# Kernel tuning notes

Hardware: AMD Instinct MI355X
Metric: run time of the kernel (lower is better)

## Reference

```python
import jax, jax.numpy as jnp
import numpy as np

N, E, IN_FEATS, D, H, DIST_DIM, NBOUND = 10000, 160000, 128, 64, 4, 32, 31

def setup_inputs() -> dict:
    key = jax.random.key(0)
    ks = jax.random.split(key, 16)
    gain = 5.0 / 3.0  # tanh gain
    def xavier(k, shape):
        # xavier_normal over the last two dims (fan_in, fan_out) as torch does per-slice
        fan_in, fan_out = shape[-2], shape[-1]
        std = gain * np.sqrt(2.0 / (fan_in + fan_out))
        return jax.random.normal(k, shape, dtype=jnp.float32) * std
    inp = {
        'feat': jax.random.normal(ks[0], (N, IN_FEATS), dtype=jnp.float32),
        'locations': jax.random.normal(ks[1], (N, 3), dtype=jnp.float32),
        'src': jax.random.randint(ks[2], (E,), 0, N),
        'dst': jax.random.randint(ks[3], (E,), 0, N),
        'inter_ids': jax.random.randint(ks[4], (E, H), 0, N),
        'W_fc': xavier(ks[5], (IN_FEATS, H * D)),
        'embed_table': jax.random.normal(ks[6], (NBOUND + 1, DIST_DIM), dtype=jnp.float32),
        'G': xavier(ks[7], (H, DIST_DIM, D)),
        'attn_fc1': xavier(ks[8], (H, 2 * D, D)),
        'attn_fc2': xavier(ks[9], (H, 2 * D, D)),
        'attn_fc3': xavier(ks[10], (H, 2 * D, D)),
        'attn_fc': xavier(ks[11], (H, 3 * D, D)),
        'attn_out': xavier(ks[12], (H, D, 1)),
        'boundaries': jnp.linspace(0.1, 3.1, NBOUND).astype(jnp.float32),
    }
    return inp


def reference(feat, locations, W_fc, embed_table, G, attn_fc1, attn_fc2, attn_fc3,
              attn_fc, attn_out, boundaries, src, dst, inter_ids):
    n = feat.shape[0]
    h = (feat @ W_fc).reshape(n, H, D)                      # [N,H,D]
    pos = locations                                          # [N,3]
    src_pos = pos[src]                                       # [E,3]
    dst_pos = pos[dst]                                       # [E,3]
    inter_pos = pos[inter_ids]                               # [E,H,3]
    h_src = h[src]                                           # [E,H,D]
    h_dst = h[dst]                                           # [E,H,D]
    head_idx = jnp.arange(H)[None, :]
    inter_h = h[inter_ids, head_idx, :]                      # [E,H,D] per-head gather

    e_count = src.shape[0]
    dist1 = jnp.broadcast_to(jnp.linalg.norm(dst_pos - src_pos, axis=-1)[:, None], (e_count, H))
    dist2 = jnp.linalg.norm(dst_pos[:, None, :] - inter_pos, axis=-1)   # [E,H]
    dist_ = jnp.linalg.norm(src_pos[:, None, :] - inter_pos, axis=-1)   # [E,H]

    def dist_embed(dist):
        idx = jnp.searchsorted(boundaries, dist, side='left')  # torch.bucketize(right=False)
        e = embed_table[idx]                                   # [E,H,DIST_DIM]
        return jnp.einsum('ehk,hkd->ehd', e, G)                # [E,H,D]

    de1 = dist_embed(dist1)
    de2 = dist_embed(dist2)
    de_ = dist_embed(dist_)

    d1 = jnp.einsum('ehk,hkd->ehd', jnp.concatenate([h_src, de1], axis=-1), attn_fc1)
    d2 = jnp.einsum('ehk,hkd->ehd', jnp.concatenate([inter_h, de2], axis=-1), attn_fc2)
    d3 = jnp.einsum('ehk,hkd->ehd', jnp.concatenate([h_dst, de_], axis=-1), attn_fc3)

    h_c = jnp.tanh(jnp.einsum('ehk,hkd->ehd', jnp.concatenate([d1, d2, d3], axis=-1), attn_fc))
    e_score = jnp.einsum('ehd,hdo->eho', h_c, attn_out)[..., 0]        # [E,H]

    # edge softmax grouped by destination node
    m = jax.ops.segment_max(e_score, dst, num_segments=n)              # [N,H]
    ex = jnp.exp(e_score - m[dst])
    den = jax.ops.segment_sum(ex, dst, num_segments=n)                 # [N,H]
    a = ex / den[dst]                                                  # [E,H]

    ft = jax.ops.segment_sum(a[:, :, None] * h_src, dst, num_segments=n)  # [N,H,D]
    rst = jnp.mean(ft, axis=1)                                          # merge='mean' -> [N,D]
    return rst
```

## Files before the change

### kernel.cpp

```cpp
#include <hip/hip_runtime.h>
#include <hip/hip_fp16.h>
#include <math.h>

#define N_NODES 10000
#define E_EDGES 160000
#define DMODEL 64
#define H 4
#define NBOUND 31
#define QREC 1024

typedef _Float16 half8 __attribute__((ext_vector_type(8)));
typedef float floatx4 __attribute__((ext_vector_type(4)));

__global__ __launch_bounds__(256) void prep_pre1_cvt_kernel(
    const float* __restrict__ fc1, const float* __restrict__ fc2,
    const float* __restrict__ fc3, const float* __restrict__ fcc,
    float* __restrict__ Bws, const float* __restrict__ pos,
    float4* __restrict__ pos4, int* __restrict__ counts,
    const float* __restrict__ feat, __half* __restrict__ feat16) {
  __shared__ __align__(16) float S[12288];
  int bi = blockIdx.x;
  int tid = threadIdx.x;
  if (bi >= 52) {
    int t = (bi - 52) * 256 + tid;
    float4 v = *(const float4*)(feat + t * 4);
    union { uint2 u; __half2 h[2]; } st;
    st.h[0] = __floats2half2_rn(v.x, v.y);
    st.h[1] = __floats2half2_rn(v.z, v.w);
    *(uint2*)&feat16[t * 4] = st.u;
    return;
  }
  if (bi >= 12) {
    int n = (bi - 12) * 256 + tid;
    if (n < N_NODES) {
      counts[n] = 0;
      pos4[n] = make_float4(pos[n * 3], pos[n * 3 + 1], pos[n * 3 + 2], 0.f);
    }
    return;
  }
  int kh = bi;
  int k = kh >> 2, h = kh & 3;
  const float* fck = (k == 0) ? fc1 : (k == 1) ? fc2 : fc3;
  fck += h * 128 * 64;
  const float* F = fcc + h * 192 * 64 + k * 64 * 64;
  #pragma unroll
  for (int u = 0; u < 8; ++u)
    ((float4*)S)[u * 256 + tid] = ((const float4*)fck)[u * 256 + tid];
  #pragma unroll
  for (int u = 0; u < 4; ++u)
    ((float4*)(S + 8192))[u * 256 + tid] = ((const float4*)F)[u * 256 + tid];
  __syncthreads();
  int j = tid & 63, ig = tid >> 6;
  #pragma unroll
  for (int rg = 0; rg < 8; ++rg) {
    int i0 = ig * 32 + rg * 4;
    float a0 = 0.f, a1 = 0.f, a2 = 0.f, a3 = 0.f;
    #pragma unroll
    for (int t4 = 0; t4 < 16; ++t4) {
      float4 f0 = *(const float4*)&S[(i0 + 0) * 64 + t4 * 4];
      float4 f1 = *(const float4*)&S[(i0 + 1) * 64 + t4 * 4];
      float4 f2 = *(const float4*)&S[(i0 + 2) * 64 + t4 * 4];
      float4 f3 = *(const float4*)&S[(i0 + 3) * 64 + t4 * 4];
      float b0 = S[8192 + (t4 * 4 + 0) * 64 + j];
      float b1 = S[8192 + (t4 * 4 + 1) * 64 + j];
      float b2 = S[8192 + (t4 * 4 + 2) * 64 + j];
      float b3 = S[8192 + (t4 * 4 + 3) * 64 + j];
      a0 += f0.x * b0 + f0.y * b1 + f0.z * b2 + f0.w * b3;
      a1 += f1.x * b0 + f1.y * b1 + f1.z * b2 + f1.w * b3;
      a2 += f2.x * b0 + f2.y * b1 + f2.z * b2 + f2.w * b3;
      a3 += f3.x * b0 + f3.y * b1 + f3.z * b2 + f3.w * b3;
    }
    Bws[kh * 8192 + (i0 + 0) * 64 + j] = a0;
    Bws[kh * 8192 + (i0 + 1) * 64 + j] = a1;
    Bws[kh * 8192 + (i0 + 2) * 64 + j] = a2;
    Bws[kh * 8192 + (i0 + 3) * 64 + j] = a3;
  }
}

__device__ __forceinline__ int didx(const float* __restrict__ bnd2, float d) {
  int g = (int)(d * 10.0f);
  g = (g < 0) ? 0 : ((g > 31) ? 31 : g);
  g += (bnd2[g + 1] < d) ? 1 : 0;
  g -= (bnd2[g] >= d) ? 1 : 0;
  return g;
}

__device__ __forceinline__ void dist_one(
    const float* __restrict__ S, const int* __restrict__ src,
    const int* __restrict__ dst, const int* __restrict__ inter,
    const float4* __restrict__ pos4, int* __restrict__ counts,
    int* __restrict__ widx, int g) {
  int e = g >> 2, h = g & 3;
  int s = src[e], t = dst[e];
  int it = inter[g];
  float4 ps = pos4[s], pt = pos4[t], pi = pos4[it];
  float dx = pt.x - ps.x, dy = pt.y - ps.y, dz = pt.z - ps.z;
  float dist1 = sqrtf(dx * dx + dy * dy + dz * dz);
  float ax = pt.x - pi.x, ay = pt.y - pi.y, az = pt.z - pi.z;
  float dist2 = sqrtf(ax * ax + ay * ay + az * az);
  float bx = ps.x - pi.x, by = ps.y - pi.y, bz = ps.z - pi.z;
  float dist_ = sqrtf(bx * bx + by * by + bz * bz);
  int idx1 = didx(S, dist1);
  int idx2 = didx(S, dist2);
  int idx_ = didx(S, dist_);
  widx[g] = idx1 | (idx2 << 5) | (idx_ << 10);
  if (h == 0) atomicAdd(&counts[t], 1);
}

__global__ __launch_bounds__(256) void pre2_dist_kernel(
    const float* __restrict__ Wfc, const float* __restrict__ G,
    const float* __restrict__ emb, const float* __restrict__ Bws,
    __half* __restrict__ bigWT, __half* __restrict__ U16,
    const int* __restrict__ src, const int* __restrict__ dst,
    const int* __restrict__ inter, const float4* __restrict__ pos4,
    const float* __restrict__ boundaries, int* __restrict__ counts,
    int* __restrict__ widx) {
  __shared__ __align__(16) float S[9216];
  int bi = blockIdx.x;
  int tid = threadIdx.x;
  if (bi >= 60) {
    if (tid < NBOUND) S[tid + 1] = boundaries[tid];
    if (tid == NBOUND) { S[0] = -INFINITY; S[32] = INFINITY; }
    __syncthreads();
    int g0 = (bi - 60) * 512 + tid;
    dist_one(S, src, dst, inter, pos4, counts, widx, g0);
    dist_one(S, src, dst, inter, pos4, counts, widx, g0 + 256);
    return;
  }
  int kh = bi / 5, role = bi % 5;
  int k = kh >> 2, h = kh & 3;
  int j = tid & 63;
  if (role < 4) {
    int r0 = role * 32;
    #pragma unroll
    for (int u = 0; u < 4; ++u)
      ((float4*)S)[u * 256 + tid] = ((const float4*)(Bws + kh * 8192))[u * 256 + tid];
    #pragma unroll
    for (int u = 0; u < 2; ++u) {
      int fi = u * 256 + tid;
      int i = fi >> 4, c4 = fi & 15;
      ((float4*)(S + 4096))[fi] =
          ((const float4*)(Wfc + (r0 + i) * 256 + h * 64))[c4];
    }
    __syncthreads();
    int ig = tid >> 6;
    int i0 = ig * 8;
    #pragma unroll
    for (int g4 = 0; g4 < 2; ++g4) {
      int ib = i0 + g4 * 4;
      float a0 = 0.f, a1 = 0.f, a2 = 0.f, a3 = 0.f;
      #pragma unroll
      for (int t4 = 0; t4 < 16; ++t4) {
        float4 f0 = *(const float4*)&S[4096 + (ib + 0) * 64 + t4 * 4];
        float4 f1 = *(const float4*)&S[4096 + (ib + 1) * 64 + t4 * 4];
        float4 f2 = *(const float4*)&S[4096 + (ib + 2) * 64 + t4 * 4];
        float4 f3 = *(const float4*)&S[4096 + (ib + 3) * 64 + t4 * 4];
        float b0 = S[(t4 * 4 + 0) * 64 + j];
        float b1 = S[(t4 * 4 + 1) * 64 + j];
        float b2 = S[(t4 * 4 + 2) * 64 + j];
        float b3 = S[(t4 * 4 + 3) * 64 + j];
        a0 += f0.x * b0 + f0.y * b1 + f0.z * b2 + f0.w * b3;
        a1 += f1.x * b0 + f1.y * b1 + f1.z * b2 + f1.w * b3;
        a2 += f2.x * b0 + f2.y * b1 + f2.z * b2 + f2.w * b3;
        a3 += f3.x * b0 + f3.y * b1 + f3.z * b2 + f3.w * b3;
      }
      __half hv[4] = {__float2half(a0), __float2half(a1), __float2half(a2),
                      __float2half(a3)};
      *(uint2*)&bigWT[((k + 1) * 256 + h * 64 + j) * 128 + r0 + ib] =
          *(uint2*)hv;
    }
    if (k == 0) {
      #pragma unroll
      for (int u = 0; u < 8; ++u) {
        int idx = u * 256 + tid;
        int i = idx >> 6, jj = idx & 63;
        bigWT[(h * 64 + jj) * 128 + r0 + i] = __float2half(S[4096 + idx]);
      }
    }
  } else {
    #pragma unroll
    for (int u = 0; u < 4; ++u)
      ((float4*)S)[u * 256 + tid] =
          ((const float4*)(Bws + kh * 8192 + 4096))[u * 256 + tid];
    #pragma unroll
    for (int u = 0; u < 2; ++u)
      ((float4*)(S + 4096))[u * 256 + tid] =
          ((const float4*)(G + h * 2048))[u * 256 + tid];
    ((float4*)(S + 6144))[tid] = ((const float4*)emb)[tid];
    __syncthreads();
    int wv = tid >> 6;
    #pragma unroll
    for (int rg = 0; rg < 2; ++rg) {
      int g0 = wv * 8 + rg * 4;
      float a0 = 0.f, a1 = 0.f, a2 = 0.f, a3 = 0.f;
      #pragma unroll
      for (int t4 = 0; t4 < 16; ++t4) {
        float4 f0 = *(const float4*)&S[4096 + (g0 + 0) * 64 + t4 * 4];
        float4 f1 = *(const float4*)&S[4096 + (g0 + 1) * 64 + t4 * 4];
        float4 f2 = *(const float4*)&S[4096 + (g0 + 2) * 64 + t4 * 4];
        float4 f3 = *(const float4*)&S[4096 + (g0 + 3) * 64 + t4 * 4];
        float b0 = S[(t4 * 4 + 0) * 64 + j];
        float b1 = S[(t4 * 4 + 1) * 64 + j];
        float b2 = S[(t4 * 4 + 2) * 64 + j];
        float b3 = S[(t4 * 4 + 3) * 64 + j];
        a0 += f0.x * b0 + f0.y * b1 + f0.z * b2 + f0.w * b3;
        a1 += f1.x * b0 + f1.y * b1 + f1.z * b2 + f1.w * b3;
        a2 += f2.x * b0 + f2.y * b1 + f2.z * b2 + f2.w * b3;
        a3 += f3.x * b0 + f3.y * b1 + f3.z * b2 + f3.w * b3;
      }
      S[7168 + (g0 + 0) * 64 + j] = a0;
      S[7168 + (g0 + 1) * 64 + j] = a1;
      S[7168 + (g0 + 2) * 64 + j] = a2;
      S[7168 + (g0 + 3) * 64 + j] = a3;
    }
    __syncthreads();
    #pragma unroll
    for (int rg = 0; rg < 2; ++rg) {
      int e0 = wv * 8 + rg * 4;
      float a0 = 0.f, a1 = 0.f, a2 = 0.f, a3 = 0.f;
      #pragma unroll
      for (int t4 = 0; t4 < 8; ++t4) {
        float4 f0 = *(const float4*)&S[6144 + (e0 + 0) * 32 + t4 * 4];
        float4 f1 = *(const float4*)&S[6144 + (e0 + 1) * 32 + t4 * 4];
        float4 f2 = *(const float4*)&S[6144 + (e0 + 2) * 32 + t4 * 4];
        float4 f3 = *(const float4*)&S[6144 + (e0 + 3) * 32 + t4 * 4];
        float b0 = S[7168 + (t4 * 4 + 0) * 64 + j];
        float b1 = S[7168 + (t4 * 4 + 1) * 64 + j];
        float b2 = S[7168 + (t4 * 4 + 2) * 64 + j];
        float b3 = S[7168 + (t4 * 4 + 3) * 64 + j];
        a0 += f0.x * b0 + f0.y * b1 + f0.z * b2 + f0.w * b3;
        a1 += f1.x * b0 + f1.y * b1 + f1.z * b2 + f1.w * b3;
        a2 += f2.x * b0 + f2.y * b1 + f2.z * b2 + f2.w * b3;
        a3 += f3.x * b0 + f3.y * b1 + f3.z * b2 + f3.w * b3;
      }
      int base = k * 8192 + h * 2048;
      U16[base + (e0 + 0) * 64 + j] = __float2half(a0);
      U16[base + (e0 + 1) * 64 + j] = __float2half(a1);
      U16[base + (e0 + 2) * 64 + j] = __float2half(a2);
      U16[base + (e0 + 3) * 64 + j] = __float2half(a3);
    }
  }
}

#define EROW 264

__global__ __launch_bounds__(256) void scan_gemm_kernel(
    const int* __restrict__ counts, int* __restrict__ starts,
    int* __restrict__ cursor, const __half* __restrict__ feat16,
    const __half* __restrict__ bigWT, __half* __restrict__ qall) {
  int bi = blockIdx.x;
  int tid = threadIdx.x;
  if (bi == 0) {
    __shared__ int lds[256];
    int base = tid * 40;
    int loc[40];
    int s = 0;
    #pragma unroll
    for (int u = 0; u < 40; ++u) {
      int i = base + u;
      int v = (i < N_NODES) ? counts[i] : 0;
      loc[u] = s;
      s += v;
    }
    lds[tid] = s;
    __syncthreads();
    int inc = s;
    for (int off = 1; off < 256; off <<= 1) {
      int y = (tid >= off) ? lds[tid - off] : 0;
      __syncthreads();
      inc += y;
      lds[tid] = inc;
      __syncthreads();
    }
    int excl = inc - s;
    #pragma unroll
    for (int u = 0; u < 40; ++u) {
      int i = base + u;
      if (i < N_NODES) {
        int v = excl + loc[u];
        starts[i] = v;
        cursor[i] = v;
      }
    }
    if (tid == 255) starts[N_NODES] = inc;
    return;
  }
  __shared__ __align__(16) __half Esm[4][16][EROW];
  int gb = bi - 1;
  int bx = gb % 157, by = gb / 157;
  int wv = tid >> 6, l = tid & 63;
  int m0 = bx * 64 + wv * 16;
  int n0 = by * 256;
  int lm = l & 15, lk = (l >> 4) * 8;
  int arow = m0 + lm;
  if (arow >= N_NODES) arow = N_NODES - 1;
  const _Float16* fp = (const _Float16*)feat16 + arow * 128 + lk;
  const _Float16* bp = (const _Float16*)bigWT + lk;
  half8 a[4];
  #pragma unroll
  for (int kt = 0; kt < 4; ++kt) a[kt] = *(const half8*)(fp + kt * 32);
  #pragma unroll
  for (int nt = 0; nt < 16; ++nt) {
    floatx4 acc = (floatx4){0.f, 0.f, 0.f, 0.f};
    #pragma unroll
    for (int kt = 0; kt < 4; ++kt) {
      half8 b = *(const half8*)(bp + (n0 + nt * 16 + lm) * 128 + kt * 32);
      acc = __builtin_amdgcn_mfma_f32_16x16x32_f16(a[kt], b, acc, 0, 0, 0);
    }
    int dd = nt * 16 + lm;
    int o = (by == 0) ? ((dd & 63) * 4 + (dd >> 6)) : dd;
    #pragma unroll
    for (int r4 = 0; r4 < 4; ++r4) {
      Esm[wv][(l >> 4) * 4 + r4][o] = __float2half(acc[r4]);
    }
  }
  __syncthreads();
  int row = l >> 2;
  int j0 = (l & 3) * 64;
  int m = m0 + row;
  if (m < N_NODES) {
    #pragma unroll
    for (int u = 0; u < 8; ++u) {
      uint4 v = *(const uint4*)&Esm[wv][row][j0 + u * 8];
      *(uint4*)&qall[m * QREC + by * 256 + j0 + u * 8] = v;
    }
  }
}

__device__ __forceinline__ float dpp_row_sum16(float v) {
  int x;
  x = __builtin_amdgcn_update_dpp(0, __float_as_int(v), 0x128, 0xf, 0xf, true);
  v += __int_as_float(x);
  x = __builtin_amdgcn_update_dpp(0, __float_as_int(v), 0x124, 0xf, 0xf, true);
  v += __int_as_float(x);
  x = __builtin_amdgcn_update_dpp(0, __float_as_int(v), 0x122, 0xf, 0xf, true);
  v += __int_as_float(x);
  x = __builtin_amdgcn_update_dpp(0, __float_as_int(v), 0x121, 0xf, 0xf, true);
  v += __int_as_float(x);
  return v;
}

union H4u { uint2 u; __half2 h[2]; };

__device__ __forceinline__ float tanh_dot(H4u A, H4u B, H4u C, H4u X, H4u Y,
                                          H4u Z, float4 a4) {
  __half2 z0 = __hadd2(__hadd2(A.h[0], B.h[0]), __hadd2(C.h[0], X.h[0]));
  z0 = __hadd2(z0, __hadd2(Y.h[0], Z.h[0]));
  __half2 z1 = __hadd2(__hadd2(A.h[1], B.h[1]), __hadd2(C.h[1], X.h[1]));
  z1 = __hadd2(z1, __hadd2(Y.h[1], Z.h[1]));
  float2 f0 = __half22float2(z0);
  float2 f1 = __half22float2(z1);
  const float K = 2.885390082f;
  float p0 = __builtin_amdgcn_exp2f(f0.x * K);
  float p1 = __builtin_amdgcn_exp2f(f0.y * K);
  float p2 = __builtin_amdgcn_exp2f(f1.x * K);
  float p3 = __builtin_amdgcn_exp2f(f1.y * K);
  float r0 = __builtin_amdgcn_rcpf(p0 + 1.0f);
  float r1 = __builtin_amdgcn_rcpf(p1 + 1.0f);
  float r2 = __builtin_amdgcn_rcpf(p2 + 1.0f);
  float r3 = __builtin_amdgcn_rcpf(p3 + 1.0f);
  float dot = a4.x * r0;
  dot = fmaf(a4.y, r1, dot);
  dot = fmaf(a4.z, r2, dot);
  dot = fmaf(a4.w, r3, dot);
  float asum = (a4.x + a4.y) + (a4.z + a4.w);
  return fmaf(-2.0f, dot, asum);
}

__global__ __launch_bounds__(256) void score_fill_kernel(
    const int* __restrict__ src, const int* __restrict__ dst,
    const int* __restrict__ inter, const int* __restrict__ widx,
    const __half* __restrict__ qall, const __half* __restrict__ U16,
    const float* __restrict__ aout, int* __restrict__ cursor,
    float* __restrict__ exsc, int* __restrict__ esrc) {
  int tid = threadIdx.x;
  int wv = tid >> 6, lane = tid & 63;
  int h = lane >> 4, c = lane & 15;
  int e0 = blockIdx.x * 8 + wv * 2;
  int e1 = e0 + 1;
  int s0 = src[e0], t0 = dst[e0];
  int s1 = src[e1], t1 = dst[e1];
  int it0 = inter[e0 * 4 + h], it1 = inter[e1 * 4 + h];
  int wp0 = widx[e0 * 4 + h], wp1 = widx[e1 * 4 + h];
  int i10 = wp0 & 31, i20 = (wp0 >> 5) & 31, i_0 = (wp0 >> 10) & 31;
  int i11 = wp1 & 31, i21 = (wp1 >> 5) & 31, i_1 = (wp1 >> 10) & 31;
  H4u A0, B0, C0, X0, Y0, Z0, A1, B1, C1, X1, Y1, Z1;
  A0.u = *(const uint2*)(qall + s0 * QREC + 256 + h * 64 + c * 4);
  A1.u = *(const uint2*)(qall + s1 * QREC + 256 + h * 64 + c * 4);
  B0.u = *(const uint2*)(qall + it0 * QREC + 512 + h * 64 + c * 4);
  B1.u = *(const uint2*)(qall + it1 * QREC + 512 + h * 64 + c * 4);
  C0.u = *(const uint2*)(qall + t0 * QREC + 768 + h * 64 + c * 4);
  C1.u = *(const uint2*)(qall + t1 * QREC + 768 + h * 64 + c * 4);
  X0.u = *(const uint2*)(U16 + (h * 32 + i10) * 64 + c * 4);
  X1.u = *(const uint2*)(U16 + (h * 32 + i11) * 64 + c * 4);
  Y0.u = *(const uint2*)(U16 + 8192 + (h * 32 + i20) * 64 + c * 4);
  Y1.u = *(const uint2*)(U16 + 8192 + (h * 32 + i21) * 64 + c * 4);
  Z0.u = *(const uint2*)(U16 + 16384 + (h * 32 + i_0) * 64 + c * 4);
  Z1.u = *(const uint2*)(U16 + 16384 + (h * 32 + i_1) * 64 + c * 4);
  const float4 a4 = *((const float4*)(aout + h * 64) + c);
  float v0 = tanh_dot(A0, B0, C0, X0, Y0, Z0, a4);
  float v1 = tanh_dot(A1, B1, C1, X1, Y1, Z1, a4);
  v0 = dpp_row_sum16(v0);
  v1 = dpp_row_sum16(v1);
  int p0 = 0, p1 = 0;
  if (lane == 0) {
    p0 = atomicAdd(&cursor[t0], 1);
    p1 = atomicAdd(&cursor[t1], 1);
  }
  p0 = __shfl(p0, 0);
  p1 = __shfl(p1, 0);
  if (c == 0) {
    exsc[p0 * 4 + h] = __expf(v0);
    exsc[p1 * 4 + h] = __expf(v1);
  }
  if (lane == 0) {
    esrc[p0] = s0;
    esrc[p1] = s1;
  }
}

__device__ __forceinline__ float4 h4_to_f4(uint2 u) {
  union { uint2 ui; __half2 h[2]; } cc;
  cc.ui = u;
  float2 a = __half22float2(cc.h[0]);
  float2 b = __half22float2(cc.h[1]);
  return make_float4(a.x, a.y, b.x, b.y);
}

__global__ __launch_bounds__(256) void agg_kernel(
    const int* __restrict__ starts, const int* __restrict__ esrc,
    const float* __restrict__ exsc, const __half* __restrict__ qall,
    float* __restrict__ out) {
  __shared__ float4 sm_num[4][64];
  __shared__ float4 sm_den[4];
  int tid = threadIdx.x;
  int w = tid >> 6, lane = tid & 63;
  int n = blockIdx.x;
  int b = starts[n], e_end = starts[n + 1];
  float4 num = make_float4(0.f, 0.f, 0.f, 0.f);
  float4 den = make_float4(0.f, 0.f, 0.f, 0.f);
  int i = b + w;
  while (i < e_end) {
    float4 ex[4];
    uint2 hr[4];
    #pragma unroll
    for (int u = 0; u < 4; ++u) {
      ex[u] = make_float4(0.f, 0.f, 0.f, 0.f);
      hr[u] = make_uint2(0, 0);
      int idx = i + u * 4;
      if (idx < e_end) {
        ex[u] = *(const float4*)(exsc + idx * 4);
        hr[u] = *(const uint2*)(qall + esrc[idx] * QREC + lane * 4);
      }
    }
    #pragma unroll
    for (int u = 0; u < 4; ++u) {
      float4 hv = h4_to_f4(hr[u]);
      num.x += ex[u].x * hv.x;
      num.y += ex[u].y * hv.y;
      num.z += ex[u].z * hv.z;
      num.w += ex[u].w * hv.w;
      den.x += ex[u].x; den.y += ex[u].y; den.z += ex[u].z; den.w += ex[u].w;
    }
    i += 16;
  }
  sm_num[w][lane] = num;
  if (lane == 0) sm_den[w] = den;
  __syncthreads();
  if (tid < 64) {
    float4 n0 = sm_num[0][tid], n1 = sm_num[1][tid];
    float4 n2 = sm_num[2][tid], n3 = sm_num[3][tid];
    float4 d0 = sm_den[0], d1 = sm_den[1], d2 = sm_den[2], d3 = sm_den[3];
    float4 ns = make_float4(n0.x + n1.x + n2.x + n3.x, n0.y + n1.y + n2.y + n3.y,
                            n0.z + n1.z + n2.z + n3.z, n0.w + n1.w + n2.w + n3.w);
    float4 ds = make_float4(d0.x + d1.x + d2.x + d3.x, d0.y + d1.y + d2.y + d3.y,
                            d0.z + d1.z + d2.z + d3.z, d0.w + d1.w + d2.w + d3.w);
    float r = 0.f;
    if (e_end > b)
      r = 0.25f * (ns.x / ds.x + ns.y / ds.y + ns.z / ds.z + ns.w / ds.w);
    out[n * 64 + tid] = r;
  }
}

extern "C" void kernel_launch(void* const* d_in, const int* in_sizes, int n_in,
                              void* d_out, int out_size, void* d_ws,
                              size_t ws_size, hipStream_t stream) {
  const float* feat = (const float*)d_in[0];
  const float* loc = (const float*)d_in[1];
  const int* src = (const int*)d_in[2];
  const int* dst = (const int*)d_in[3];
  const int* inter = (const int*)d_in[4];
  const float* Wfc = (const float*)d_in[5];
  const float* emb = (const float*)d_in[6];
  const float* G = (const float*)d_in[7];
  const float* fc1 = (const float*)d_in[8];
  const float* fc2 = (const float*)d_in[9];
  const float* fc3 = (const float*)d_in[10];
  const float* fcc = (const float*)d_in[11];
  const float* aout = (const float*)d_in[12];
  const float* bnd = (const float*)d_in[13];
  float* out = (float*)d_out;

  __half* qall = (__half*)d_ws;
  __half* bigWT = qall + N_NODES * QREC;
  __half* U16 = bigWT + 1024 * 128;
  __half* feat16 = U16 + 3 * H * 2048;
  float* Bws = (float*)(feat16 + N_NODES * 128);
  float4* pos4 = (float4*)(Bws + 12 * 8192);
  float* exsc = (float*)(pos4 + N_NODES);
  int* widx = (int*)(exsc + E_EDGES * 4);
  int* counts = widx + E_EDGES * 4;
  int* starts = counts + N_NODES;
  int* cursor = starts + N_NODES + 1;
  int* esrc = cursor + N_NODES;

  prep_pre1_cvt_kernel<<<1302, 256, 0, stream>>>(fc1, fc2, fc3, fcc, Bws, loc,
                                                 pos4, counts, feat, feat16);
  pre2_dist_kernel<<<60 + 1250, 256, 0, stream>>>(
      Wfc, G, emb, Bws, bigWT, U16, src, dst, inter, pos4, bnd, counts, widx);
  scan_gemm_kernel<<<1 + 157 * 4, 256, 0, stream>>>(counts, starts, cursor,
                                                    feat16, bigWT, qall);
  score_fill_kernel<<<E_EDGES / 8, 256, 0, stream>>>(
      src, dst, inter, widx, qall, U16, aout, cursor, exsc, esrc);
  agg_kernel<<<N_NODES, 256, 0, stream>>>(starts, esrc, exsc, qall, out);
}
```

Measured before the change: 209.7 us.

## Merge prep kernels, build dst histogram in scan block, widen score and agg per-wave work

Folds the two weight-precompute kernels and the distance-bucket kernel into one launch. Each of the 12 weight blocks now computes its whole fused weight chain in shared memory, so the Bws intermediate and pos4 staging buffer go away. Destination counts move out of global atomics into a single-block shared-memory histogram inside the scan, which serializes 160k atomics on one block. The score kernel handles 4 edges per wave instead of 2 for more memory-level parallelism. The aggregation kernel assigns one node per wave, dropping the cross-wave shared-memory reduction and barrier.

```diff
diff --git a/kernel.cpp b/kernel.cpp
--- a/kernel.cpp
+++ b/kernel.cpp
@@ -12,17 +12,76 @@
 typedef _Float16 half8 __attribute__((ext_vector_type(8)));
 typedef float floatx4 __attribute__((ext_vector_type(4)));
 
-__global__ __launch_bounds__(256) void prep_pre1_cvt_kernel(
+__device__ __forceinline__ void mm4(const float* __restrict__ S, int aoff,
+                                    int astride, int boff, int i0, int j,
+                                    int Kdim, float o[4]) {
+  float a0 = 0.f, a1 = 0.f, a2 = 0.f, a3 = 0.f;
+  for (int t4 = 0; t4 < (Kdim >> 2); ++t4) {
+    float4 f0 = *(const float4*)&S[aoff + (i0 + 0) * astride + t4 * 4];
+    float4 f1 = *(const float4*)&S[aoff + (i0 + 1) * astride + t4 * 4];
+    float4 f2 = *(const float4*)&S[aoff + (i0 + 2) * astride + t4 * 4];
+    float4 f3 = *(const float4*)&S[aoff + (i0 + 3) * astride + t4 * 4];
+    float b0 = S[boff + (t4 * 4 + 0) * 64 + j];
+    float b1 = S[boff + (t4 * 4 + 1) * 64 + j];
+    float b2 = S[boff + (t4 * 4 + 2) * 64 + j];
+    float b3 = S[boff + (t4 * 4 + 3) * 64 + j];
+    a0 += f0.x * b0 + f0.y * b1 + f0.z * b2 + f0.w * b3;
+    a1 += f1.x * b0 + f1.y * b1 + f1.z * b2 + f1.w * b3;
+    a2 += f2.x * b0 + f2.y * b1 + f2.z * b2 + f2.w * b3;
+    a3 += f3.x * b0 + f3.y * b1 + f3.z * b2 + f3.w * b3;
+  }
+  o[0] = a0; o[1] = a1; o[2] = a2; o[3] = a3;
+}
+
+__device__ __forceinline__ int didx(const float* __restrict__ bnd2, float d) {
+  int g = (int)(d * 10.0f);
+  g = (g < 0) ? 0 : ((g > 31) ? 31 : g);
+  g += (bnd2[g + 1] < d) ? 1 : 0;
+  g -= (bnd2[g] >= d) ? 1 : 0;
+  return g;
+}
+
+__global__ __launch_bounds__(256) void prep_kernel(
     const float* __restrict__ fc1, const float* __restrict__ fc2,
     const float* __restrict__ fc3, const float* __restrict__ fcc,
-    float* __restrict__ Bws, const float* __restrict__ pos,
-    float4* __restrict__ pos4, int* __restrict__ counts,
-    const float* __restrict__ feat, __half* __restrict__ feat16) {
+    const float* __restrict__ Wfc, const float* __restrict__ G,
+    const float* __restrict__ emb, const float* __restrict__ feat,
+    const float* __restrict__ pos, const int* __restrict__ src,
+    const int* __restrict__ dst, const int* __restrict__ inter,
+    const float* __restrict__ boundaries, __half* __restrict__ bigWT,
+    __half* __restrict__ U16, __half* __restrict__ feat16,
+    int* __restrict__ widx) {
   __shared__ __align__(16) float S[12288];
   int bi = blockIdx.x;
   int tid = threadIdx.x;
-  if (bi >= 52) {
-    int t = (bi - 52) * 256 + tid;
+  if (bi >= 1262) {
+    if (tid < NBOUND) S[tid + 1] = boundaries[tid];
+    if (tid == NBOUND) { S[0] = -INFINITY; S[32] = INFINITY; }
+    __syncthreads();
+    #pragma unroll
+    for (int rep = 0; rep < 2; ++rep) {
+      int g = (bi - 1262) * 512 + rep * 256 + tid;
+      int e = g >> 2;
+      int s = src[e], t = dst[e];
+      int it = inter[g];
+      float sx = pos[s * 3], sy = pos[s * 3 + 1], sz = pos[s * 3 + 2];
+      float tx = pos[t * 3], ty = pos[t * 3 + 1], tz = pos[t * 3 + 2];
+      float ix = pos[it * 3], iy = pos[it * 3 + 1], iz = pos[it * 3 + 2];
+      float dx = tx - sx, dy = ty - sy, dz = tz - sz;
+      float dist1 = sqrtf(dx * dx + dy * dy + dz * dz);
+      float ax = tx - ix, ay = ty - iy, az = tz - iz;
+      float dist2 = sqrtf(ax * ax + ay * ay + az * az);
+      float bx = sx - ix, by = sy - iy, bz = sz - iz;
+      float dist_ = sqrtf(bx * bx + by * by + bz * bz);
+      int idx1 = didx(S, dist1);
+      int idx2 = didx(S, dist2);
+      int idx_ = didx(S, dist_);
+      widx[g] = idx1 | (idx2 << 5) | (idx_ << 10);
+    }
+    return;
+  }
+  if (bi >= 12) {
+    int t = (bi - 12) * 256 + tid;
     float4 v = *(const float4*)(feat + t * 4);
     union { uint2 u; __half2 h[2]; } st;
     st.h[0] = __floats2half2_rn(v.x, v.y);
@@ -30,262 +89,169 @@
     *(uint2*)&feat16[t * 4] = st.u;
     return;
   }
-  if (bi >= 12) {
-    int n = (bi - 12) * 256 + tid;
-    if (n < N_NODES) {
-      counts[n] = 0;
-      pos4[n] = make_float4(pos[n * 3], pos[n * 3 + 1], pos[n * 3 + 2], 0.f);
-    }
-    return;
-  }
-  int kh = bi;
-  int k = kh >> 2, h = kh & 3;
+  int k = bi >> 2, h = bi & 3;
   const float* fck = (k == 0) ? fc1 : (k == 1) ? fc2 : fc3;
   fck += h * 128 * 64;
   const float* F = fcc + h * 192 * 64 + k * 64 * 64;
-  #pragma unroll
-  for (int u = 0; u < 8; ++u)
-    ((float4*)S)[u * 256 + tid] = ((const float4*)fck)[u * 256 + tid];
+  int j = tid & 63, ig = tid >> 6;
+  float o[4];
+  #pragma unroll
+  for (int u = 0; u < 4; ++u) {
+    ((float4*)S)[u * 256 + tid] = ((const float4*)F)[u * 256 + tid];
+    ((float4*)(S + 4096))[u * 256 + tid] = ((const float4*)fck)[u * 256 + tid];
+  }
+  __syncthreads();
+  #pragma unroll
+  for (int rg = 0; rg < 4; ++rg) {
+    int i0 = ig * 16 + rg * 4;
+    mm4(S, 4096, 64, 0, i0, j, 64, o);
+    S[8192 + (i0 + 0) * 64 + j] = o[0];
+    S[8192 + (i0 + 1) * 64 + j] = o[1];
+    S[8192 + (i0 + 2) * 64 + j] = o[2];
+    S[8192 + (i0 + 3) * 64 + j] = o[3];
+  }
+  __syncthreads();
+  #pragma unroll
+  for (int u = 0; u < 4; ++u) {
+    int fi = u * 256 + tid;
+    int i = fi >> 4, c4 = fi & 15;
+    ((float4*)(S + 4096))[fi] = ((const float4*)(Wfc + i * 256 + h * 64))[c4];
+  }
+  __syncthreads();
+  if (k == 0) {
+    #pragma unroll
+    for (int u = 0; u < 16; ++u) {
+      int idx = u * 256 + tid;
+      int i = idx >> 6, jj = idx & 63;
+      bigWT[(h * 64 + jj) * 128 + i] = __float2half(S[4096 + idx]);
+    }
+  }
+  #pragma unroll
+  for (int rg = 0; rg < 4; ++rg) {
+    int i0 = ig * 16 + rg * 4;
+    mm4(S, 4096, 64, 8192, i0, j, 64, o);
+    int rb = ((k + 1) * 256 + h * 64 + j) * 128;
+    bigWT[rb + i0 + 0] = __float2half(o[0]);
+    bigWT[rb + i0 + 1] = __float2half(o[1]);
+    bigWT[rb + i0 + 2] = __float2half(o[2]);
+    bigWT[rb + i0 + 3] = __float2half(o[3]);
+  }
+  __syncthreads();
+  #pragma unroll
+  for (int u = 0; u < 4; ++u) {
+    int fi = u * 256 + tid;
+    int i = fi >> 4, c4 = fi & 15;
+    ((float4*)(S + 4096))[fi] =
+        ((const float4*)(Wfc + (64 + i) * 256 + h * 64))[c4];
+  }
+  __syncthreads();
+  if (k == 0) {
+    #pragma unroll
+    for (int u = 0; u < 16; ++u) {
+      int idx = u * 256 + tid;
+      int i = idx >> 6, jj = idx & 63;
+      bigWT[(h * 64 + jj) * 128 + 64 + i] = __float2half(S[4096 + idx]);
+    }
+  }
+  #pragma unroll
+  for (int rg = 0; rg < 4; ++rg) {
+    int i0 = ig * 16 + rg * 4;
+    mm4(S, 4096, 64, 8192, i0, j, 64, o);
+    int rb = ((k + 1) * 256 + h * 64 + j) * 128;
+    bigWT[rb + 64 + i0 + 0] = __float2half(o[0]);
+    bigWT[rb + 64 + i0 + 1] = __float2half(o[1]);
+    bigWT[rb + 64 + i0 + 2] = __float2half(o[2]);
+    bigWT[rb + 64 + i0 + 3] = __float2half(o[3]);
+  }
+  __syncthreads();
   #pragma unroll
   for (int u = 0; u < 4; ++u)
-    ((float4*)(S + 8192))[u * 256 + tid] = ((const float4*)F)[u * 256 + tid];
-  __syncthreads();
-  int j = tid & 63, ig = tid >> 6;
-  #pragma unroll
-  for (int rg = 0; rg < 8; ++rg) {
-    int i0 = ig * 32 + rg * 4;
-    float a0 = 0.f, a1 = 0.f, a2 = 0.f, a3 = 0.f;
-    #pragma unroll
-    for (int t4 = 0; t4 < 16; ++t4) {
-      float4 f0 = *(const float4*)&S[(i0 + 0) * 64 + t4 * 4];
-      float4 f1 = *(const float4*)&S[(i0 + 1) * 64 + t4 * 4];
-      float4 f2 = *(const float4*)&S[(i0 + 2) * 64 + t4 * 4];
-      float4 f3 = *(const float4*)&S[(i0 + 3) * 64 + t4 * 4];
-      float b0 = S[8192 + (t4 * 4 + 0) * 64 + j];
-      float b1 = S[8192 + (t4 * 4 + 1) * 64 + j];
-      float b2 = S[8192 + (t4 * 4 + 2) * 64 + j];
-      float b3 = S[8192 + (t4 * 4 + 3) * 64 + j];
-      a0 += f0.x * b0 + f0.y * b1 + f0.z * b2 + f0.w * b3;
-      a1 += f1.x * b0 + f1.y * b1 + f1.z * b2 + f1.w * b3;
-      a2 += f2.x * b0 + f2.y * b1 + f2.z * b2 + f2.w * b3;
-      a3 += f3.x * b0 + f3.y * b1 + f3.z * b2 + f3.w * b3;
-    }
-    Bws[kh * 8192 + (i0 + 0) * 64 + j] = a0;
-    Bws[kh * 8192 + (i0 + 1) * 64 + j] = a1;
-    Bws[kh * 8192 + (i0 + 2) * 64 + j] = a2;
-    Bws[kh * 8192 + (i0 + 3) * 64 + j] = a3;
-  }
-}
-
-__device__ __forceinline__ int didx(const float* __restrict__ bnd2, float d) {
-  int g = (int)(d * 10.0f);
-  g = (g < 0) ? 0 : ((g > 31) ? 31 : g);
-  g += (bnd2[g + 1] < d) ? 1 : 0;
-  g -= (bnd2[g] >= d) ? 1 : 0;
-  return g;
-}
-
-__device__ __forceinline__ void dist_one(
-    const float* __restrict__ S, const int* __restrict__ src,
-    const int* __restrict__ dst, const int* __restrict__ inter,
-    const float4* __restrict__ pos4, int* __restrict__ counts,
-    int* __restrict__ widx, int g) {
-  int e = g >> 2, h = g & 3;
-  int s = src[e], t = dst[e];
-  int it = inter[g];
-  float4 ps = pos4[s], pt = pos4[t], pi = pos4[it];
-  float dx = pt.x - ps.x, dy = pt.y - ps.y, dz = pt.z - ps.z;
-  float dist1 = sqrtf(dx * dx + dy * dy + dz * dz);
-  float ax = pt.x - pi.x, ay = pt.y - pi.y, az = pt.z - pi.z;
-  float dist2 = sqrtf(ax * ax + ay * ay + az * az);
-  float bx = ps.x - pi.x, by = ps.y - pi.y, bz = ps.z - pi.z;
-  float dist_ = sqrtf(bx * bx + by * by + bz * bz);
-  int idx1 = didx(S, dist1);
-  int idx2 = didx(S, dist2);
-  int idx_ = didx(S, dist_);
-  widx[g] = idx1 | (idx2 << 5) | (idx_ << 10);
-  if (h == 0) atomicAdd(&counts[t], 1);
-}
-
-__global__ __launch_bounds__(256) void pre2_dist_kernel(
-    const float* __restrict__ Wfc, const float* __restrict__ G,
-    const float* __restrict__ emb, const float* __restrict__ Bws,
-    __half* __restrict__ bigWT, __half* __restrict__ U16,
-    const int* __restrict__ src, const int* __restrict__ dst,
-    const int* __restrict__ inter, const float4* __restrict__ pos4,
-    const float* __restrict__ boundaries, int* __restrict__ counts,
-    int* __restrict__ widx) {
-  __shared__ __align__(16) float S[9216];
-  int bi = blockIdx.x;
-  int tid = threadIdx.x;
-  if (bi >= 60) {
-    if (tid < NBOUND) S[tid + 1] = boundaries[tid];
-    if (tid == NBOUND) { S[0] = -INFINITY; S[32] = INFINITY; }
-    __syncthreads();
-    int g0 = (bi - 60) * 512 + tid;
-    dist_one(S, src, dst, inter, pos4, counts, widx, g0);
-    dist_one(S, src, dst, inter, pos4, counts, widx, g0 + 256);
-    return;
-  }
-  int kh = bi / 5, role = bi % 5;
-  int k = kh >> 2, h = kh & 3;
-  int j = tid & 63;
-  if (role < 4) {
-    int r0 = role * 32;
-    #pragma unroll
-    for (int u = 0; u < 4; ++u)
-      ((float4*)S)[u * 256 + tid] = ((const float4*)(Bws + kh * 8192))[u * 256 + tid];
-    #pragma unroll
-    for (int u = 0; u < 2; ++u) {
-      int fi = u * 256 + tid;
-      int i = fi >> 4, c4 = fi & 15;
-      ((float4*)(S + 4096))[fi] =
-          ((const float4*)(Wfc + (r0 + i) * 256 + h * 64))[c4];
-    }
-    __syncthreads();
-    int ig = tid >> 6;
-    int i0 = ig * 8;
-    #pragma unroll
-    for (int g4 = 0; g4 < 2; ++g4) {
-      int ib = i0 + g4 * 4;
-      float a0 = 0.f, a1 = 0.f, a2 = 0.f, a3 = 0.f;
-      #pragma unroll
-      for (int t4 = 0; t4 < 16; ++t4) {
-        float4 f0 = *(const float4*)&S[4096 + (ib + 0) * 64 + t4 * 4];
-        float4 f1 = *(const float4*)&S[4096 + (ib + 1) * 64 + t4 * 4];
-        float4 f2 = *(const float4*)&S[4096 + (ib + 2) * 64 + t4 * 4];
-        float4 f3 = *(const float4*)&S[4096 + (ib + 3) * 64 + t4 * 4];
-        float b0 = S[(t4 * 4 + 0) * 64 + j];
-        float b1 = S[(t4 * 4 + 1) * 64 + j];
-        float b2 = S[(t4 * 4 + 2) * 64 + j];
-        float b3 = S[(t4 * 4 + 3) * 64 + j];
-        a0 += f0.x * b0 + f0.y * b1 + f0.z * b2 + f0.w * b3;
-        a1 += f1.x * b0 + f1.y * b1 + f1.z * b2 + f1.w * b3;
-        a2 += f2.x * b0 + f2.y * b1 + f2.z * b2 + f2.w * b3;
-        a3 += f3.x * b0 + f3.y * b1 + f3.z * b2 + f3.w * b3;
-      }
-      __half hv[4] = {__float2half(a0), __float2half(a1), __float2half(a2),
-                      __float2half(a3)};
-      *(uint2*)&bigWT[((k + 1) * 256 + h * 64 + j) * 128 + r0 + ib] =
-          *(uint2*)hv;
-    }
-    if (k == 0) {
-      #pragma unroll
-      for (int u = 0; u < 8; ++u) {
-        int idx = u * 256 + tid;
-        int i = idx >> 6, jj = idx & 63;
-        bigWT[(h * 64 + jj) * 128 + r0 + i] = __float2half(S[4096 + idx]);
-      }
-    }
-  } else {
-    #pragma unroll
-    for (int u = 0; u < 4; ++u)
-      ((float4*)S)[u * 256 + tid] =
-          ((const float4*)(Bws + kh * 8192 + 4096))[u * 256 + tid];
-    #pragma unroll
-    for (int u = 0; u < 2; ++u)
-      ((float4*)(S + 4096))[u * 256 + tid] =
-          ((const float4*)(G + h * 2048))[u * 256 + tid];
-    ((float4*)(S + 6144))[tid] = ((const float4*)emb)[tid];
-    __syncthreads();
-    int wv = tid >> 6;
-    #pragma unroll
-    for (int rg = 0; rg < 2; ++rg) {
-      int g0 = wv * 8 + rg * 4;
-      float a0 = 0.f, a1 = 0.f, a2 = 0.f, a3 = 0.f;
-      #pragma unroll
-      for (int t4 = 0; t4 < 16; ++t4) {
-        float4 f0 = *(const float4*)&S[4096 + (g0 + 0) * 64 + t4 * 4];
-        float4 f1 = *(const float4*)&S[4096 + (g0 + 1) * 64 + t4 * 4];
-        float4 f2 = *(const float4*)&S[4096 + (g0 + 2) * 64 + t4 * 4];
-        float4 f3 = *(const float4*)&S[4096 + (g0 + 3) * 64 + t4 * 4];
-        float b0 = S[(t4 * 4 + 0) * 64 + j];
-        float b1 = S[(t4 * 4 + 1) * 64 + j];
-        float b2 = S[(t4 * 4 + 2) * 64 + j];
-        float b3 = S[(t4 * 4 + 3) * 64 + j];
-        a0 += f0.x * b0 + f0.y * b1 + f0.z * b2 + f0.w * b3;
-        a1 += f1.x * b0 + f1.y * b1 + f1.z * b2 + f1.w * b3;
-        a2 += f2.x * b0 + f2.y * b1 + f2.z * b2 + f2.w * b3;
-        a3 += f3.x * b0 + f3.y * b1 + f3.z * b2 + f3.w * b3;
-      }
-      S[7168 + (g0 + 0) * 64 + j] = a0;
-      S[7168 + (g0 + 1) * 64 + j] = a1;
-      S[7168 + (g0 + 2) * 64 + j] = a2;
-      S[7168 + (g0 + 3) * 64 + j] = a3;
-    }
-    __syncthreads();
-    #pragma unroll
-    for (int rg = 0; rg < 2; ++rg) {
-      int e0 = wv * 8 + rg * 4;
-      float a0 = 0.f, a1 = 0.f, a2 = 0.f, a3 = 0.f;
-      #pragma unroll
-      for (int t4 = 0; t4 < 8; ++t4) {
-        float4 f0 = *(const float4*)&S[6144 + (e0 + 0) * 32 + t4 * 4];
-        float4 f1 = *(const float4*)&S[6144 + (e0 + 1) * 32 + t4 * 4];
-        float4 f2 = *(const float4*)&S[6144 + (e0 + 2) * 32 + t4 * 4];
-        float4 f3 = *(const float4*)&S[6144 + (e0 + 3) * 32 + t4 * 4];
-        float b0 = S[7168 + (t4 * 4 + 0) * 64 + j];
-        float b1 = S[7168 + (t4 * 4 + 1) * 64 + j];
-        float b2 = S[7168 + (t4 * 4 + 2) * 64 + j];
-        float b3 = S[7168 + (t4 * 4 + 3) * 64 + j];
-        a0 += f0.x * b0 + f0.y * b1 + f0.z * b2 + f0.w * b3;
-        a1 += f1.x * b0 + f1.y * b1 + f1.z * b2 + f1.w * b3;
-        a2 += f2.x * b0 + f2.y * b1 + f2.z * b2 + f2.w * b3;
-        a3 += f3.x * b0 + f3.y * b1 + f3.z * b2 + f3.w * b3;
-      }
-      int base = k * 8192 + h * 2048;
-      U16[base + (e0 + 0) * 64 + j] = __float2half(a0);
-      U16[base + (e0 + 1) * 64 + j] = __float2half(a1);
-      U16[base + (e0 + 2) * 64 + j] = __float2half(a2);
-      U16[base + (e0 + 3) * 64 + j] = __float2half(a3);
-    }
+    ((float4*)(S + 4096))[u * 256 + tid] =
+        ((const float4*)(fck + 4096))[u * 256 + tid];
+  __syncthreads();
+  #pragma unroll
+  for (int rg = 0; rg < 4; ++rg) {
+    int i0 = ig * 16 + rg * 4;
+    mm4(S, 4096, 64, 0, i0, j, 64, o);
+    S[8192 + (i0 + 0) * 64 + j] = o[0];
+    S[8192 + (i0 + 1) * 64 + j] = o[1];
+    S[8192 + (i0 + 2) * 64 + j] = o[2];
+    S[8192 + (i0 + 3) * 64 + j] = o[3];
+  }
+  __syncthreads();
+  #pragma unroll
+  for (int u = 0; u < 2; ++u)
+    ((float4*)S)[u * 256 + tid] = ((const float4*)(G + h * 2048))[u * 256 + tid];
+  ((float4*)(S + 2048))[tid] = ((const float4*)emb)[tid];
+  __syncthreads();
+  #pragma unroll
+  for (int rg = 0; rg < 2; ++rg) {
+    int i0 = ig * 8 + rg * 4;
+    mm4(S, 0, 64, 8192, i0, j, 64, o);
+    S[3072 + (i0 + 0) * 64 + j] = o[0];
+    S[3072 + (i0 + 1) * 64 + j] = o[1];
+    S[3072 + (i0 + 2) * 64 + j] = o[2];
+    S[3072 + (i0 + 3) * 64 + j] = o[3];
+  }
+  __syncthreads();
+  #pragma unroll
+  for (int rg = 0; rg < 2; ++rg) {
+    int i0 = ig * 8 + rg * 4;
+    mm4(S, 2048, 32, 3072, i0, j, 32, o);
+    int base = k * 8192 + h * 2048;
+    U16[base + (i0 + 0) * 64 + j] = __float2half(o[0]);
+    U16[base + (i0 + 1) * 64 + j] = __float2half(o[1]);
+    U16[base + (i0 + 2) * 64 + j] = __float2half(o[2]);
+    U16[base + (i0 + 3) * 64 + j] = __float2half(o[3]);
   }
 }
 
 #define EROW 264
 
 __global__ __launch_bounds__(256) void scan_gemm_kernel(
-    const int* __restrict__ counts, int* __restrict__ starts,
-    int* __restrict__ cursor, const __half* __restrict__ feat16,
-    const __half* __restrict__ bigWT, __half* __restrict__ qall) {
+    const int* __restrict__ dst, const __half* __restrict__ feat16,
+    const __half* __restrict__ bigWT, __half* __restrict__ qall,
+    int* __restrict__ starts, int* __restrict__ cursor) {
+  __shared__ __align__(16) char SMEM[42112];
   int bi = blockIdx.x;
   int tid = threadIdx.x;
   if (bi == 0) {
-    __shared__ int lds[256];
+    int* hist = (int*)SMEM;
+    int* part = hist + 10240;
+    #pragma unroll
+    for (int u = 0; u < 40; ++u) hist[u * 256 + tid] = 0;
+    __syncthreads();
+    for (int u = 0; u < 625; ++u) atomicAdd(&hist[dst[u * 256 + tid]], 1);
+    __syncthreads();
     int base = tid * 40;
-    int loc[40];
     int s = 0;
-    #pragma unroll
     for (int u = 0; u < 40; ++u) {
       int i = base + u;
-      int v = (i < N_NODES) ? counts[i] : 0;
-      loc[u] = s;
-      s += v;
-    }
-    lds[tid] = s;
+      if (i < N_NODES) s += hist[i];
+    }
+    part[tid] = s;
     __syncthreads();
     int inc = s;
     for (int off = 1; off < 256; off <<= 1) {
-      int y = (tid >= off) ? lds[tid - off] : 0;
+      int y = (tid >= off) ? part[tid - off] : 0;
       __syncthreads();
       inc += y;
-      lds[tid] = inc;
+      part[tid] = inc;
       __syncthreads();
     }
-    int excl = inc - s;
-    #pragma unroll
+    int run = inc - s;
     for (int u = 0; u < 40; ++u) {
       int i = base + u;
       if (i < N_NODES) {
-        int v = excl + loc[u];
-        starts[i] = v;
-        cursor[i] = v;
+        starts[i] = run;
+        cursor[i] = run;
+        run += hist[i];
       }
     }
     if (tid == 255) starts[N_NODES] = inc;
     return;
   }
-  __shared__ __align__(16) __half Esm[4][16][EROW];
+  auto Esm = (__half(*)[16][EROW])SMEM;
   int gb = bi - 1;
   int bx = gb % 157, by = gb / 157;
   int wv = tid >> 6, l = tid & 63;
@@ -310,9 +276,8 @@
     int dd = nt * 16 + lm;
     int o = (by == 0) ? ((dd & 63) * 4 + (dd >> 6)) : dd;
     #pragma unroll
-    for (int r4 = 0; r4 < 4; ++r4) {
+    for (int r4 = 0; r4 < 4; ++r4)
       Esm[wv][(l >> 4) * 4 + r4][o] = __float2half(acc[r4]);
-    }
   }
   __syncthreads();
   int row = l >> 2;
@@ -376,46 +341,48 @@
   int tid = threadIdx.x;
   int wv = tid >> 6, lane = tid & 63;
   int h = lane >> 4, c = lane & 15;
-  int e0 = blockIdx.x * 8 + wv * 2;
-  int e1 = e0 + 1;
-  int s0 = src[e0], t0 = dst[e0];
-  int s1 = src[e1], t1 = dst[e1];
-  int it0 = inter[e0 * 4 + h], it1 = inter[e1 * 4 + h];
-  int wp0 = widx[e0 * 4 + h], wp1 = widx[e1 * 4 + h];
-  int i10 = wp0 & 31, i20 = (wp0 >> 5) & 31, i_0 = (wp0 >> 10) & 31;
-  int i11 = wp1 & 31, i21 = (wp1 >> 5) & 31, i_1 = (wp1 >> 10) & 31;
-  H4u A0, B0, C0, X0, Y0, Z0, A1, B1, C1, X1, Y1, Z1;
-  A0.u = *(const uint2*)(qall + s0 * QREC + 256 + h * 64 + c * 4);
-  A1.u = *(const uint2*)(qall + s1 * QREC + 256 + h * 64 + c * 4);
-  B0.u = *(const uint2*)(qall + it0 * QREC + 512 + h * 64 + c * 4);
-  B1.u = *(const uint2*)(qall + it1 * QREC + 512 + h * 64 + c * 4);
-  C0.u = *(const uint2*)(qall + t0 * QREC + 768 + h * 64 + c * 4);
-  C1.u = *(const uint2*)(qall + t1 * QREC + 768 + h * 64 + c * 4);
-  X0.u = *(const uint2*)(U16 + (h * 32 + i10) * 64 + c * 4);
-  X1.u = *(const uint2*)(U16 + (h * 32 + i11) * 64 + c * 4);
-  Y0.u = *(const uint2*)(U16 + 8192 + (h * 32 + i20) * 64 + c * 4);
-  Y1.u = *(const uint2*)(U16 + 8192 + (h * 32 + i21) * 64 + c * 4);
-  Z0.u = *(const uint2*)(U16 + 16384 + (h * 32 + i_0) * 64 + c * 4);
-  Z1.u = *(const uint2*)(U16 + 16384 + (h * 32 + i_1) * 64 + c * 4);
+  int e0 = blockIdx.x * 16 + wv * 4;
+  int s_[4], t_[4], it_[4], wp_[4];
+  #pragma unroll
+  for (int q = 0; q < 4; ++q) {
+    int e = e0 + q;
+    s_[q] = src[e];
+    t_[q] = dst[e];
+    it_[q] = inter[e * 4 + h];
+    wp_[q] = widx[e * 4 + h];
+  }
+  H4u A[4], B[4], C[4], X[4], Y[4], Z[4];
+  #pragma unroll
+  for (int q = 0; q < 4; ++q) {
+    A[q].u = *(const uint2*)(qall + s_[q] * QREC + 256 + h * 64 + c * 4);
+    B[q].u = *(const uint2*)(qall + it_[q] * QREC + 512 + h * 64 + c * 4);
+    C[q].u = *(const uint2*)(qall + t_[q] * QREC + 768 + h * 64 + c * 4);
+    int i1 = wp_[q] & 31, i2 = (wp_[q] >> 5) & 31, i3 = (wp_[q] >> 10) & 31;
+    X[q].u = *(const uint2*)(U16 + (h * 32 + i1) * 64 + c * 4);
+    Y[q].u = *(const uint2*)(U16 + 8192 + (h * 32 + i2) * 64 + c * 4);
+    Z[q].u = *(const uint2*)(U16 + 16384 + (h * 32 + i3) * 64 + c * 4);
+  }
   const float4 a4 = *((const float4*)(aout + h * 64) + c);
-  float v0 = tanh_dot(A0, B0, C0, X0, Y0, Z0, a4);
-  float v1 = tanh_dot(A1, B1, C1, X1, Y1, Z1, a4);
-  v0 = dpp_row_sum16(v0);
-  v1 = dpp_row_sum16(v1);
-  int p0 = 0, p1 = 0;
+  float v[4];
+  #pragma unroll
+  for (int q = 0; q < 4; ++q)
+    v[q] = tanh_dot(A[q], B[q], C[q], X[q], Y[q], Z[q], a4);
+  #pragma unroll
+  for (int q = 0; q < 4; ++q) v[q] = dpp_row_sum16(v[q]);
+  int p[4] = {0, 0, 0, 0};
   if (lane == 0) {
-    p0 = atomicAdd(&cursor[t0], 1);
-    p1 = atomicAdd(&cursor[t1], 1);
-  }
-  p0 = __shfl(p0, 0);
-  p1 = __shfl(p1, 0);
+    #pragma unroll
+    for (int q = 0; q < 4; ++q) p[q] = atomicAdd(&cursor[t_[q]], 1);
+  }
+  #pragma unroll
+  for (int q = 0; q < 4; ++q) p[q] = __shfl(p[q], 0);
   if (c == 0) {
-    exsc[p0 * 4 + h] = __expf(v0);
-    exsc[p1 * 4 + h] = __expf(v1);
+    #pragma unroll
+    for (int q = 0; q < 4; ++q) exsc[p[q] * 4 + h] = __expf(v[q]);
   }
   if (lane == 0) {
-    esrc[p0] = s0;
-    esrc[p1] = s1;
+    #pragma unroll
+    for (int q = 0; q < 4; ++q) esrc[p[q]] = s_[q];
   }
 }
 
@@ -431,55 +398,42 @@
     const int* __restrict__ starts, const int* __restrict__ esrc,
     const float* __restrict__ exsc, const __half* __restrict__ qall,
     float* __restrict__ out) {
-  __shared__ float4 sm_num[4][64];
-  __shared__ float4 sm_den[4];
   int tid = threadIdx.x;
   int w = tid >> 6, lane = tid & 63;
-  int n = blockIdx.x;
+  int n = blockIdx.x * 4 + w;
   int b = starts[n], e_end = starts[n + 1];
   float4 num = make_float4(0.f, 0.f, 0.f, 0.f);
   float4 den = make_float4(0.f, 0.f, 0.f, 0.f);
-  int i = b + w;
-  while (i < e_end) {
-    float4 ex[4];
-    uint2 hr[4];
-    #pragma unroll
-    for (int u = 0; u < 4; ++u) {
+  for (int i = b; i < e_end; i += 8) {
+    float4 ex[8];
+    uint2 hr[8];
+    #pragma unroll
+    for (int u = 0; u < 8; ++u) {
       ex[u] = make_float4(0.f, 0.f, 0.f, 0.f);
       hr[u] = make_uint2(0, 0);
-      int idx = i + u * 4;
+      int idx = i + u;
       if (idx < e_end) {
         ex[u] = *(const float4*)(exsc + idx * 4);
         hr[u] = *(const uint2*)(qall + esrc[idx] * QREC + lane * 4);
       }
     }
     #pragma unroll
-    for (int u = 0; u < 4; ++u) {
+    for (int u = 0; u < 8; ++u) {
       float4 hv = h4_to_f4(hr[u]);
       num.x += ex[u].x * hv.x;
       num.y += ex[u].y * hv.y;
       num.z += ex[u].z * hv.z;
       num.w += ex[u].w * hv.w;
-      den.x += ex[u].x; den.y += ex[u].y; den.z += ex[u].z; den.w += ex[u].w;
-    }
-    i += 16;
-  }
-  sm_num[w][lane] = num;
-  if (lane == 0) sm_den[w] = den;
-  __syncthreads();
-  if (tid < 64) {
-    float4 n0 = sm_num[0][tid], n1 = sm_num[1][tid];
-    float4 n2 = sm_num[2][tid], n3 = sm_num[3][tid];
-    float4 d0 = sm_den[0], d1 = sm_den[1], d2 = sm_den[2], d3 = sm_den[3];
-    float4 ns = make_float4(n0.x + n1.x + n2.x + n3.x, n0.y + n1.y + n2.y + n3.y,
-                            n0.z + n1.z + n2.z + n3.z, n0.w + n1.w + n2.w + n3.w);
-    float4 ds = make_float4(d0.x + d1.x + d2.x + d3.x, d0.y + d1.y + d2.y + d3.y,
-                            d0.z + d1.z + d2.z + d3.z, d0.w + d1.w + d2.w + d3.w);
-    float r = 0.f;
-    if (e_end > b)
-      r = 0.25f * (ns.x / ds.x + ns.y / ds.y + ns.z / ds.z + ns.w / ds.w);
-    out[n * 64 + tid] = r;
-  }
+      den.x += ex[u].x;
+      den.y += ex[u].y;
+      den.z += ex[u].z;
+      den.w += ex[u].w;
+    }
+  }
+  float r = 0.f;
+  if (e_end > b)
+    r = 0.25f * (num.x / den.x + num.y / den.y + num.z / den.z + num.w / den.w);
+  out[n * 64 + lane] = r;
 }
 
 extern "C" void kernel_launch(void* const* d_in, const int* in_sizes, int n_in,
@@ -505,22 +459,18 @@
   __half* bigWT = qall + N_NODES * QREC;
   __half* U16 = bigWT + 1024 * 128;
   __half* feat16 = U16 + 3 * H * 2048;
-  float* Bws = (float*)(feat16 + N_NODES * 128);
-  float4* pos4 = (float4*)(Bws + 12 * 8192);
-  float* exsc = (float*)(pos4 + N_NODES);
+  float* exsc = (float*)(feat16 + N_NODES * 128);
   int* widx = (int*)(exsc + E_EDGES * 4);
-  int* counts = widx + E_EDGES * 4;
-  int* starts = counts + N_NODES;
+  int* starts = widx + E_EDGES * 4;
   int* cursor = starts + N_NODES + 1;
   int* esrc = cursor + N_NODES;
 
-  prep_pre1_cvt_kernel<<<1302, 256, 0, stream>>>(fc1, fc2, fc3, fcc, Bws, loc,
-                                                 pos4, counts, feat, feat16);
-  pre2_dist_kernel<<<60 + 1250, 256, 0, stream>>>(
-      Wfc, G, emb, Bws, bigWT, U16, src, dst, inter, pos4, bnd, counts, widx);
-  scan_gemm_kernel<<<1 + 157 * 4, 256, 0, stream>>>(counts, starts, cursor,
-                                                    feat16, bigWT, qall);
-  score_fill_kernel<<<E_EDGES / 8, 256, 0, stream>>>(
+  prep_kernel<<<2512, 256, 0, stream>>>(fc1, fc2, fc3, fcc, Wfc, G, emb, feat,
+                                        loc, src, dst, inter, bnd, bigWT, U16,
+                                        feat16, widx);
+  scan_gemm_kernel<<<1 + 157 * 4, 256, 0, stream>>>(dst, feat16, bigWT, qall,
+                                                    starts, cursor);
+  score_fill_kernel<<<E_EDGES / 16, 256, 0, stream>>>(
       src, dst, inter, widx, qall, U16, aout, cursor, exsc, esrc);
-  agg_kernel<<<N_NODES, 256, 0, stream>>>(starts, esrc, exsc, qall, out);
-}
+  agg_kernel<<<N_NODES / 4, 256, 0, stream>>>(starts, esrc, exsc, qall, out);
+}
```

Measured after the change: 366.1 us. +74.6%, slower.
